# Optimization experiments

Measured on AMD Instinct MI355X. Metric: run time of the kernel, lower is better.

Reference implementation:

```python
import jax, jax.numpy as jnp
import numpy as np

B, LAT, D = 64, 256, 64           # batch, latent dim, voxel grid side (== output image side)
ALPHA_ADJ = float(np.log2(D) + 2)  # alpha_adjust = log2(output_img_shape[0]) + 2


def _rotmat(a):
    """3x3 rotation matrix from Euler angles (x,y,z), R = Rz @ Ry @ Rx."""
    cx, sx = jnp.cos(a[0]), jnp.sin(a[0])
    cy, sy = jnp.cos(a[1]), jnp.sin(a[1])
    cz, sz = jnp.cos(a[2]), jnp.sin(a[2])
    Rx = jnp.array([[1, 0, 0], [0, 0, 0], [0, 0, 0]], jnp.float32).at[1, 1].set(cx).at[1, 2].set(-sx).at[2, 1].set(sx).at[2, 2].set(cx)
    Ry = jnp.array([[0, 0, 0], [0, 1, 0], [0, 0, 0]], jnp.float32).at[0, 0].set(cy).at[0, 2].set(sy).at[2, 0].set(-sy).at[2, 2].set(cy)
    Rz = jnp.array([[0, 0, 0], [0, 0, 0], [0, 0, 1]], jnp.float32).at[0, 0].set(cz).at[0, 1].set(-sz).at[1, 0].set(sz).at[1, 1].set(cz)
    return Rz @ Ry @ Rx


def _apply_transform(vol, R):
    """Rotate a [D,D,D] volume about its centre via trilinear sampling, zero padding."""
    d = vol.shape[0]
    c = (d - 1) / 2.0
    idx = jnp.arange(d, dtype=jnp.float32)
    gi, gj, gk = jnp.meshgrid(idx, idx, idx, indexing='ij')
    dst = jnp.stack([gi, gj, gk], axis=-1) - c        # [D,D,D,3]
    src = dst @ R.T + c                                # source coords
    x, y, z = src[..., 0], src[..., 1], src[..., 2]
    x0 = jnp.floor(x); y0 = jnp.floor(y); z0 = jnp.floor(z)
    fx, fy, fz = x - x0, y - y0, z - z0

    def gather(ix, iy, iz):
        valid = (ix >= 0) & (ix < d) & (iy >= 0) & (iy < d) & (iz >= 0) & (iz < d)
        ixc = jnp.clip(ix, 0, d - 1).astype(jnp.int32)
        iyc = jnp.clip(iy, 0, d - 1).astype(jnp.int32)
        izc = jnp.clip(iz, 0, d - 1).astype(jnp.int32)
        return jnp.where(valid, vol[ixc, iyc, izc], 0.0)

    c000 = gather(x0, y0, z0);     c001 = gather(x0, y0, z0 + 1)
    c010 = gather(x0, y0 + 1, z0); c011 = gather(x0, y0 + 1, z0 + 1)
    c100 = gather(x0 + 1, y0, z0); c101 = gather(x0 + 1, y0, z0 + 1)
    c110 = gather(x0 + 1, y0 + 1, z0); c111 = gather(x0 + 1, y0 + 1, z0 + 1)
    c00 = c000 * (1 - fz) + c001 * fz
    c01 = c010 * (1 - fz) + c011 * fz
    c10 = c100 * (1 - fz) + c101 * fz
    c11 = c110 * (1 - fz) + c111 * fz
    c0 = c00 * (1 - fy) + c01 * fy
    c1 = c10 * (1 - fy) + c11 * fy
    return c0 * (1 - fx) + c1 * fx


def setup_inputs() -> dict:
    key = jax.random.key(0)
    k1, k2, k3 = jax.random.split(key, 3)
    encoded = jax.random.normal(k1, (B, LAT), dtype=jnp.float32)
    W = jax.random.normal(k2, (LAT, D * D * D), dtype=jnp.float32) * 0.02
    b = jnp.zeros((D * D * D,), jnp.float32)
    angles = jax.random.uniform(k3, (B, 3), jnp.float32, -np.pi, np.pi)
    return {"encoded": encoded, "W": W, "b": b, "angles": angles}


def reference(encoded, W, b, angles):
    # voxel_generator: linear -> sigmoid -> [B, D, D, D], then alpha sharpening
    voxels = jax.nn.sigmoid(encoded @ W + b).reshape(B, D, D, D)
    voxels = voxels ** ALPHA_ADJ
    R = jax.vmap(_rotmat)(angles)                       # [B,3,3]
    views = jax.vmap(_apply_transform)(voxels, R)       # [B,D,D,D]
    # alpha compositing back-to-front along last (depth) axis
    alphas = jnp.moveaxis(views, -1, 0)[:, :, None]     # [Dz, B, 1, H, W]
    def step(img, a):
        return img * (1 - a) + a, None
    images, _ = jax.lax.scan(step, jnp.zeros((B, 1, D, D), jnp.float32), alphas, reverse=True)
    return 2 * images - 1
```

## Files before the change

### kernel.cpp

```cpp
#include <hip/hip_runtime.h>
#include <hip/hip_bf16.h>
#include <hip/hip_fp16.h>
#include <math.h>

#define BATCH 64
#define LAT   256
#define DVOX  64
#define VOX   (DVOX*DVOX*DVOX)

typedef __attribute__((ext_vector_type(8))) short short8;
typedef __attribute__((ext_vector_type(4))) float f32x4;

__global__ void prep_kernel(const float* __restrict__ enc,
                            const float* __restrict__ angles,
                            unsigned short* __restrict__ encB,
                            float* __restrict__ Rmat) {
    int tid = threadIdx.x;
    for (int idx = tid; idx < BATCH * LAT; idx += blockDim.x) {
        __hip_bfloat16 h = __float2bfloat16(enc[idx]);
        encB[idx] = *reinterpret_cast<unsigned short*>(&h);
    }
    if (tid < BATCH) {
        float ax = angles[tid*3+0], ay = angles[tid*3+1], az = angles[tid*3+2];
        float cx = cosf(ax), sx = sinf(ax);
        float cy = cosf(ay), sy = sinf(ay);
        float cz = cosf(az), sz = sinf(az);
        float* R = Rmat + tid * 9;
        R[0] = cz*cy;  R[1] = cz*sy*sx - sz*cx;  R[2] = cz*sy*cx + sz*sx;
        R[3] = sz*cy;  R[4] = sz*sy*sx + cz*cx;  R[5] = sz*sy*cx - cz*sx;
        R[6] = -sy;    R[7] = cy*sx;             R[8] = cy*cx;
    }
}

__global__ __launch_bounds__(256, 2) void gemm_mfma_kernel(
        const unsigned short* __restrict__ encB,
        const float* __restrict__ W,
        const float* __restrict__ bias,
        __half* __restrict__ vox) {
    int wave = threadIdx.x >> 6;
    int lane = threadIdx.x & 63;
    int l15 = lane & 15, l4 = lane >> 4;
    int n4 = blockIdx.x * 256 + wave * 64 + 4 * l15;

    f32x4 acc[4][4];
#pragma unroll
    for (int t = 0; t < 4; ++t)
#pragma unroll
        for (int mt = 0; mt < 4; ++mt) acc[t][mt] = (f32x4){0.f, 0.f, 0.f, 0.f};

    const unsigned short* ap = encB + l15 * LAT + l4 * 8;
    const float* wp = W + (size_t)(l4 * 8) * VOX + n4;

    float4 wc[8], wn[8];
#pragma unroll
    for (int j = 0; j < 8; ++j)
        wc[j] = *(const float4*)(wp + (size_t)j * VOX);

#pragma unroll
    for (int kb = 0; kb < LAT; kb += 32) {
        if (kb + 32 < LAT) {
            const float* wpn = wp + (size_t)(kb + 32) * VOX;
#pragma unroll
            for (int j = 0; j < 8; ++j)
                wn[j] = *(const float4*)(wpn + (size_t)j * VOX);
        }
        short8 a[4];
#pragma unroll
        for (int mt = 0; mt < 4; ++mt)
            a[mt] = *(const short8*)(ap + mt * 16 * LAT + kb);

        short8 bf[4];
#pragma unroll
        for (int t = 0; t < 4; ++t) {
#pragma unroll
            for (int dw = 0; dw < 4; ++dw) {
                __hip_bfloat16 lo = __float2bfloat16(wc[2 * dw][t]);
                __hip_bfloat16 hi = __float2bfloat16(wc[2 * dw + 1][t]);
                bf[t][2 * dw]     = *reinterpret_cast<short*>(&lo);
                bf[t][2 * dw + 1] = *reinterpret_cast<short*>(&hi);
            }
        }
#pragma unroll
        for (int t = 0; t < 4; ++t)
#pragma unroll
            for (int mt = 0; mt < 4; ++mt)
                acc[t][mt] = __builtin_amdgcn_mfma_f32_16x16x32_bf16(a[mt], bf[t], acc[t][mt], 0, 0, 0);
#pragma unroll
        for (int j = 0; j < 8; ++j) wc[j] = wn[j];
    }

    float4 bv = *(const float4*)(bias + n4);
#pragma unroll
    for (int mt = 0; mt < 4; ++mt) {
#pragma unroll
        for (int r = 0; r < 4; ++r) {
            int b = mt * 16 + l4 * 4 + r;
            float s[4];
#pragma unroll
            for (int t = 0; t < 4; ++t) {
                float x = acc[t][mt][r] + ((const float*)&bv)[t];
                float v = 1.f / (1.f + __expf(-x));
                v = v * v; v = v * v; v = v * v;
                s[t] = v;
            }
            __half2 h01 = __floats2half2_rn(s[0], s[1]);
            __half2 h23 = __floats2half2_rn(s[2], s[3]);
            uint2 pk;
            pk.x = *reinterpret_cast<unsigned*>(&h01);
            pk.y = *reinterpret_cast<unsigned*>(&h23);
            *reinterpret_cast<uint2*>(vox + (size_t)b * VOX + n4) = pk;
        }
    }
}

__device__ __forceinline__ float zlerp(unsigned e, float fz) {
    __half2 h = *reinterpret_cast<__half2*>(&e);
    float2 f = __half22float2(h);
    return f.x + (f.y - f.x) * fz;
}

__global__ __launch_bounds__(256) void render_lds_kernel(
        const __half* __restrict__ vox,
        const float* __restrict__ Rmat,
        float* __restrict__ out) {
    __shared__ unsigned sV[16 * 16 * 17];
    __shared__ float sT[4][64], sE[4][64];

    int bid  = blockIdx.x;
    int b    = bid & 63;
    int tile = bid >> 6;
    int t    = threadIdx.x;
    int pix  = t & 63, seg = t >> 6;
    int i0 = (tile >> 3) * 8, j0 = (tile & 7) * 8;
    int i = i0 + (pix >> 3);
    int j = j0 + (pix & 7);

    const float* Rb = Rmat + b * 9;
    float R0 = Rb[0], R1 = Rb[1], R2 = Rb[2];
    float R3 = Rb[3], R4 = Rb[4], R5 = Rb[5];
    float R6 = Rb[6], R7 = Rb[7], R8 = Rb[8];

    const float c = (DVOX - 1) * 0.5f;
    float di = (float)i - c, dj = (float)j - c;
    float xb = fmaf(R0, di, fmaf(R1, dj, c));
    float yb = fmaf(R3, di, fmaf(R4, dj, c));
    float zb = fmaf(R6, di, fmaf(R7, dj, c));

    float dic = (float)i0 + 3.5f - c;
    float djc = (float)j0 + 3.5f - c;
    float hwx = 3.5f * (fabsf(R0) + fabsf(R1) + fabsf(R2)) + 1e-3f;
    float hwy = 3.5f * (fabsf(R3) + fabsf(R4) + fabsf(R5)) + 1e-3f;
    float hwz = 3.5f * (fabsf(R6) + fabsf(R7) + fabsf(R8)) + 1e-3f;

    const unsigned short* V = (const unsigned short*)vox + (size_t)b * VOX;

    int rx = t >> 4, ry = t & 15;
    unsigned d[9];
    int xlo_n, ylo_n, zlo_n, s_n;

    auto bbox = [&](int ch) {
        float dkc = (float)(ch * 8) + 3.5f - c;
        float xc = fmaf(R0, dic, fmaf(R1, djc, fmaf(R2, dkc, c)));
        float yc = fmaf(R3, dic, fmaf(R4, djc, fmaf(R5, dkc, c)));
        float zc = fmaf(R6, dic, fmaf(R7, djc, fmaf(R8, dkc, c)));
        xlo_n = (int)floorf(xc - hwx);
        ylo_n = (int)floorf(yc - hwy);
        zlo_n = (int)floorf(zc - hwz);
        s_n   = zlo_n & ~1;
    };
    auto issue = [&]() {
        int gxc = min(max(xlo_n + rx, 0), DVOX - 1);
        int gyc = min(max(ylo_n + ry, 0), DVOX - 1);
        const unsigned* p = (const unsigned*)(V + ((gxc << 12) + (gyc << 6) + s_n));
#pragma unroll
        for (int k = 0; k < 9; ++k) d[k] = p[k];
    };

    bbox(7); issue();
    int xlo = xlo_n, ylo = ylo_n, zlo = zlo_n, s = s_n;

    float img = 0.f;
#pragma unroll 1
    for (int ch = 7; ch >= 0; --ch) {
        bool zint = (zlo >= 0) && (zlo + 17 <= DVOX);

        {
            bool rv = ((unsigned)(xlo + rx) < (unsigned)DVOX) &
                      ((unsigned)(ylo + ry) < (unsigned)DVOX);
            unsigned tt[9];
#pragma unroll
            for (int k = 0; k < 9; ++k) tt[k] = d[k];
            if (!zint) {
#pragma unroll
                for (int k = 0; k < 9; ++k) {
                    int h0 = s + 2 * k;
                    unsigned m = (((unsigned)h0 < (unsigned)DVOX) ? 0x0000FFFFu : 0u)
                               | (((unsigned)(h0 + 1) < (unsigned)DVOX) ? 0xFFFF0000u : 0u);
                    tt[k] &= m;
                }
            }
            unsigned rvm = rv ? 0xFFFFFFFFu : 0u;
#pragma unroll
            for (int k = 0; k < 9; ++k) tt[k] &= rvm;

            unsigned A[8];
#pragma unroll
            for (int m = 0; m < 8; ++m)
                A[m] = (tt[m] >> 16) | (tt[m + 1] << 16);

            unsigned* wrow = sV + t * 17;
            if (zlo & 1) {
#pragma unroll
                for (int m = 0; m < 8; ++m) {
                    wrow[2 * m]     = A[m];
                    wrow[2 * m + 1] = tt[m + 1];
                }
            } else {
#pragma unroll
                for (int m = 0; m < 8; ++m) {
                    wrow[2 * m]     = tt[m];
                    wrow[2 * m + 1] = A[m];
                }
            }
        }
        __syncthreads();

        if (ch > 0) { bbox(ch - 1); issue(); }

        float T = 1.f, E = 0.f;
        int k0 = ch * 8;
#pragma unroll
        for (int q = 1; q >= 0; --q) {
            int kk = 2 * seg + q;
            float dk = (float)(k0 + kk) - c;
            float x = fmaf(R2, dk, xb);
            float y = fmaf(R5, dk, yb);
            float z = fmaf(R8, dk, zb);

            float xf = floorf(x), yf = floorf(y), zf = floorf(z);
            float fx = x - xf, fy = y - yf, fz = z - zf;
            int xi = (int)xf - xlo;
            int yi = (int)yf - ylo;
            int zi = (int)zf - zlo;
            const unsigned* e = sV + (xi * 272 + yi * 17 + zi);

            float c00 = zlerp(e[0],   fz);
            float c01 = zlerp(e[17],  fz);
            float c10 = zlerp(e[272], fz);
            float c11 = zlerp(e[289], fz);
            float c0 = c00 + (c01 - c00) * fy;
            float c1 = c10 + (c11 - c10) * fy;
            float a  = c0  + (c1  - c0 ) * fx;

            E = E * (1.f - a) + a;
            T *= (1.f - a);
        }
        sT[seg][pix] = T;
        sE[seg][pix] = E;
        __syncthreads();

        if (seg == 0) {
            float im = img;
#pragma unroll
            for (int ss = 3; ss >= 0; --ss)
                im = fmaf(sT[ss][pix], im, sE[ss][pix]);
            img = im;
        }

        xlo = xlo_n; ylo = ylo_n; zlo = zlo_n; s = s_n;
    }

    if (seg == 0)
        out[b * (DVOX * DVOX) + i * DVOX + j] = 2.f * img - 1.f;
}

extern "C" void kernel_launch(void* const* d_in, const int* in_sizes, int n_in,
                              void* d_out, int out_size, void* d_ws, size_t ws_size,
                              hipStream_t stream) {
    const float* enc    = (const float*)d_in[0];
    const float* W      = (const float*)d_in[1];
    const float* bias   = (const float*)d_in[2];
    const float* angles = (const float*)d_in[3];
    float* out = (float*)d_out;

    char* ws = (char*)d_ws;
    unsigned short* encB = (unsigned short*)ws;
    float* Rmat          = (float*)(ws + 32768);
    __half* vox          = (__half*)(ws + 65536);

    prep_kernel<<<1, 256, 0, stream>>>(enc, angles, encB, Rmat);
    gemm_mfma_kernel<<<VOX / 256, 256, 0, stream>>>(encB, W, bias, vox);
    render_lds_kernel<<<BATCH * 64, 256, 0, stream>>>(vox, Rmat, out);
}
```

Measured before the change: 143.0 us.

## Coalesce voxel tile loads across lanes and ping-pong W prefetch in GEMM

In the render kernel, each thread used to load 9 strided dwords for one row. Now 4 adjacent lanes split each row: each lane does a uint2 load plus a cross-lane shuffle for the neighbour dword, covering 4 rows per thread, which gives coalesced global access. The next chunk's load is now issued before the barrier. The GEMM kernel replaces the wc/wn copy with A/B ping-pong buffers and uses a cheaper bit-trick bf16 conversion (add 0x8000 then perm), which differs from round-to-nearest-even on ties. These changes add shuffle and predication overhead and alter register pressure.

```diff
diff --git a/kernel.cpp b/kernel.cpp
--- a/kernel.cpp
+++ b/kernel.cpp
@@ -51,42 +51,49 @@
     const unsigned short* ap = encB + l15 * LAT + l4 * 8;
     const float* wp = W + (size_t)(l4 * 8) * VOX + n4;
 
-    float4 wc[8], wn[8];
+    float4 wA[8], wB[8];
 #pragma unroll
     for (int j = 0; j < 8; ++j)
-        wc[j] = *(const float4*)(wp + (size_t)j * VOX);
-
-#pragma unroll
-    for (int kb = 0; kb < LAT; kb += 32) {
-        if (kb + 32 < LAT) {
-            const float* wpn = wp + (size_t)(kb + 32) * VOX;
-#pragma unroll
-            for (int j = 0; j < 8; ++j)
-                wn[j] = *(const float4*)(wpn + (size_t)j * VOX);
-        }
+        wA[j] = *(const float4*)(wp + (size_t)j * VOX);
+
+    auto consume = [&](const float4* w, int kb) {
         short8 a[4];
 #pragma unroll
         for (int mt = 0; mt < 4; ++mt)
             a[mt] = *(const short8*)(ap + mt * 16 * LAT + kb);
-
         short8 bf[4];
 #pragma unroll
         for (int t = 0; t < 4; ++t) {
+            unsigned bw[4];
 #pragma unroll
             for (int dw = 0; dw < 4; ++dw) {
-                __hip_bfloat16 lo = __float2bfloat16(wc[2 * dw][t]);
-                __hip_bfloat16 hi = __float2bfloat16(wc[2 * dw + 1][t]);
-                bf[t][2 * dw]     = *reinterpret_cast<short*>(&lo);
-                bf[t][2 * dw + 1] = *reinterpret_cast<short*>(&hi);
+                unsigned u0 = __float_as_uint(((const float*)&w[2 * dw])[t])     + 0x8000u;
+                unsigned u1 = __float_as_uint(((const float*)&w[2 * dw + 1])[t]) + 0x8000u;
+                bw[dw] = __builtin_amdgcn_perm(u1, u0, 0x07060302u);
             }
+            bf[t] = *reinterpret_cast<short8*>(bw);
         }
 #pragma unroll
         for (int t = 0; t < 4; ++t)
 #pragma unroll
             for (int mt = 0; mt < 4; ++mt)
                 acc[t][mt] = __builtin_amdgcn_mfma_f32_16x16x32_bf16(a[mt], bf[t], acc[t][mt], 0, 0, 0);
-#pragma unroll
-        for (int j = 0; j < 8; ++j) wc[j] = wn[j];
+    };
+
+#pragma unroll
+    for (int kb2 = 0; kb2 < LAT; kb2 += 64) {
+        {
+            const float* q = wp + (size_t)(kb2 + 32) * VOX;
+#pragma unroll
+            for (int j = 0; j < 8; ++j) wB[j] = *(const float4*)(q + (size_t)j * VOX);
+        }
+        consume(wA, kb2);
+        if (kb2 + 64 < LAT) {
+            const float* q = wp + (size_t)(kb2 + 64) * VOX;
+#pragma unroll
+            for (int j = 0; j < 8; ++j) wA[j] = *(const float4*)(q + (size_t)j * VOX);
+        }
+        consume(wB, kb2 + 32);
     }
 
     float4 bv = *(const float4*)(bias + n4);
@@ -130,7 +137,9 @@
     int b    = bid & 63;
     int tile = bid >> 6;
     int t    = threadIdx.x;
+    int lane = t & 63;
     int pix  = t & 63, seg = t >> 6;
+    int m    = t & 3,  rq  = t >> 2;
     int i0 = (tile >> 3) * 8, j0 = (tile & 7) * 8;
     int i = i0 + (pix >> 3);
     int j = j0 + (pix & 7);
@@ -154,8 +163,7 @@
 
     const unsigned short* V = (const unsigned short*)vox + (size_t)b * VOX;
 
-    int rx = t >> 4, ry = t & 15;
-    unsigned d[9];
+    unsigned D0[4], D1[4], D2[4];
     int xlo_n, ylo_n, zlo_n, s_n;
 
     auto bbox = [&](int ch) {
@@ -169,11 +177,17 @@
         s_n   = zlo_n & ~1;
     };
     auto issue = [&]() {
-        int gxc = min(max(xlo_n + rx, 0), DVOX - 1);
-        int gyc = min(max(ylo_n + ry, 0), DVOX - 1);
-        const unsigned* p = (const unsigned*)(V + ((gxc << 12) + (gyc << 6) + s_n));
-#pragma unroll
-        for (int k = 0; k < 9; ++k) d[k] = p[k];
+#pragma unroll
+        for (int p = 0; p < 4; ++p) {
+            int r = 64 * p + rq;
+            int rx = r >> 4, ry = r & 15;
+            int gxc = min(max(xlo_n + rx, 0), DVOX - 1);
+            int gyc = min(max(ylo_n + ry, 0), DVOX - 1);
+            const unsigned* pp = (const unsigned*)V + ((gxc << 11) + (gyc << 5) + (s_n >> 1));
+            uint2 dd = *(const uint2*)(pp + 2 * m);
+            D0[p] = dd.x; D1[p] = dd.y;
+            if (m == 3) D2[p] = pp[8];
+        }
     };
 
     bbox(7); issue();
@@ -183,49 +197,38 @@
 #pragma unroll 1
     for (int ch = 7; ch >= 0; --ch) {
         bool zint = (zlo >= 0) && (zlo + 17 <= DVOX);
-
-        {
+        int  odd  = zlo & 1;
+
+#pragma unroll
+        for (int p = 0; p < 4; ++p) {
+            int r = 64 * p + rq;
+            int rx = r >> 4, ry = r & 15;
             bool rv = ((unsigned)(xlo + rx) < (unsigned)DVOX) &
                       ((unsigned)(ylo + ry) < (unsigned)DVOX);
-            unsigned tt[9];
-#pragma unroll
-            for (int k = 0; k < 9; ++k) tt[k] = d[k];
+            unsigned d0 = D0[p], d1 = D1[p];
+            unsigned dnb = __shfl(D0[p], (lane + 1) & 63);
+            unsigned dn = (m == 3) ? D2[p] : dnb;
             if (!zint) {
-#pragma unroll
-                for (int k = 0; k < 9; ++k) {
-                    int h0 = s + 2 * k;
-                    unsigned m = (((unsigned)h0 < (unsigned)DVOX) ? 0x0000FFFFu : 0u)
-                               | (((unsigned)(h0 + 1) < (unsigned)DVOX) ? 0xFFFF0000u : 0u);
-                    tt[k] &= m;
-                }
+                auto mz = [&](int off) {
+                    int h0 = s + 2 * off;
+                    return (((unsigned)h0 < (unsigned)DVOX) ? 0x0000FFFFu : 0u)
+                         | (((unsigned)(h0 + 1) < (unsigned)DVOX) ? 0xFFFF0000u : 0u);
+                };
+                d0 &= mz(2 * m); d1 &= mz(2 * m + 1); dn &= mz(2 * m + 2);
             }
             unsigned rvm = rv ? 0xFFFFFFFFu : 0u;
-#pragma unroll
-            for (int k = 0; k < 9; ++k) tt[k] &= rvm;
-
-            unsigned A[8];
-#pragma unroll
-            for (int m = 0; m < 8; ++m)
-                A[m] = (tt[m] >> 16) | (tt[m + 1] << 16);
-
-            unsigned* wrow = sV + t * 17;
-            if (zlo & 1) {
-#pragma unroll
-                for (int m = 0; m < 8; ++m) {
-                    wrow[2 * m]     = A[m];
-                    wrow[2 * m + 1] = tt[m + 1];
-                }
-            } else {
-#pragma unroll
-                for (int m = 0; m < 8; ++m) {
-                    wrow[2 * m]     = tt[m];
-                    wrow[2 * m + 1] = A[m];
-                }
-            }
-        }
+            d0 &= rvm; d1 &= rvm; dn &= rvm;
+
+            unsigned A0 = (d0 >> 16) | (d1 << 16);
+            unsigned A1 = (d1 >> 16) | (dn << 16);
+
+            unsigned* wrow = sV + r * 17 + 4 * m;
+            if (odd) { wrow[0] = A0; wrow[1] = d1; wrow[2] = A1; wrow[3] = dn; }
+            else     { wrow[0] = d0; wrow[1] = A0; wrow[2] = d1; wrow[3] = A1; }
+        }
+
+        if (ch > 0) { bbox(ch - 1); issue(); }
         __syncthreads();
-
-        if (ch > 0) { bbox(ch - 1); issue(); }
 
         float T = 1.f, E = 0.f;
         int k0 = ch * 8;
```

Result: slower. 148.9 us (+4.1%).

## Halve GEMM per-thread tile, raise occupancy, use bit-trick bf16 conversion

Applied to the files above, without the earlier changes.

The GEMM kernel now gives each thread 2 output columns instead of 4, doubling the grid and raising the launch-bounds occupancy target from 2 to 4 blocks per CU. W loads are double-buffered in two alternating register sets across an unrolled k loop. The fp32-to-bf16 conversion becomes an add-and-byte-permute round-half-up trick in place of the library conversion. The smaller tile cuts register pressure so more waves can hide the memory-bound W stream, at the cost of narrower float2 loads and re-reading the A operand more often.

```diff
diff --git a/kernel.cpp b/kernel.cpp
--- a/kernel.cpp
+++ b/kernel.cpp
@@ -32,7 +32,7 @@
     }
 }
 
-__global__ __launch_bounds__(256, 2) void gemm_mfma_kernel(
+__global__ __launch_bounds__(256, 4) void gemm_mfma_kernel(
         const unsigned short* __restrict__ encB,
         const float* __restrict__ W,
         const float* __restrict__ bias,
@@ -40,75 +40,77 @@
     int wave = threadIdx.x >> 6;
     int lane = threadIdx.x & 63;
     int l15 = lane & 15, l4 = lane >> 4;
-    int n4 = blockIdx.x * 256 + wave * 64 + 4 * l15;
-
-    f32x4 acc[4][4];
-#pragma unroll
-    for (int t = 0; t < 4; ++t)
+    int n2 = blockIdx.x * 128 + wave * 32 + 2 * l15;
+
+    f32x4 acc[2][4];
+#pragma unroll
+    for (int t = 0; t < 2; ++t)
 #pragma unroll
         for (int mt = 0; mt < 4; ++mt) acc[t][mt] = (f32x4){0.f, 0.f, 0.f, 0.f};
 
     const unsigned short* ap = encB + l15 * LAT + l4 * 8;
-    const float* wp = W + (size_t)(l4 * 8) * VOX + n4;
-
-    float4 wc[8], wn[8];
+    const float* wp = W + (size_t)(l4 * 8) * VOX + n2;
+
+    float2 wA[8], wB[8];
 #pragma unroll
     for (int j = 0; j < 8; ++j)
-        wc[j] = *(const float4*)(wp + (size_t)j * VOX);
-
-#pragma unroll
-    for (int kb = 0; kb < LAT; kb += 32) {
-        if (kb + 32 < LAT) {
-            const float* wpn = wp + (size_t)(kb + 32) * VOX;
-#pragma unroll
-            for (int j = 0; j < 8; ++j)
-                wn[j] = *(const float4*)(wpn + (size_t)j * VOX);
-        }
+        wA[j] = *(const float2*)(wp + (size_t)j * VOX);
+
+    auto consume = [&](const float2* w, int kb) {
         short8 a[4];
 #pragma unroll
         for (int mt = 0; mt < 4; ++mt)
             a[mt] = *(const short8*)(ap + mt * 16 * LAT + kb);
-
-        short8 bf[4];
-#pragma unroll
-        for (int t = 0; t < 4; ++t) {
-#pragma unroll
-            for (int dw = 0; dw < 4; ++dw) {
-                __hip_bfloat16 lo = __float2bfloat16(wc[2 * dw][t]);
-                __hip_bfloat16 hi = __float2bfloat16(wc[2 * dw + 1][t]);
-                bf[t][2 * dw]     = *reinterpret_cast<short*>(&lo);
-                bf[t][2 * dw + 1] = *reinterpret_cast<short*>(&hi);
-            }
-        }
-#pragma unroll
-        for (int t = 0; t < 4; ++t)
-#pragma unroll
-            for (int mt = 0; mt < 4; ++mt)
-                acc[t][mt] = __builtin_amdgcn_mfma_f32_16x16x32_bf16(a[mt], bf[t], acc[t][mt], 0, 0, 0);
-#pragma unroll
-        for (int j = 0; j < 8; ++j) wc[j] = wn[j];
-    }
-
-    float4 bv = *(const float4*)(bias + n4);
+        unsigned bw0[4], bw1[4];
+#pragma unroll
+        for (int dw = 0; dw < 4; ++dw) {
+            unsigned e0 = __float_as_uint(w[2 * dw].x)     + 0x8000u;
+            unsigned e1 = __float_as_uint(w[2 * dw + 1].x) + 0x8000u;
+            bw0[dw] = __builtin_amdgcn_perm(e1, e0, 0x07060302u);
+            unsigned o0 = __float_as_uint(w[2 * dw].y)     + 0x8000u;
+            unsigned o1 = __float_as_uint(w[2 * dw + 1].y) + 0x8000u;
+            bw1[dw] = __builtin_amdgcn_perm(o1, o0, 0x07060302u);
+        }
+        short8 b0 = *reinterpret_cast<short8*>(bw0);
+        short8 b1 = *reinterpret_cast<short8*>(bw1);
+#pragma unroll
+        for (int mt = 0; mt < 4; ++mt) {
+            acc[0][mt] = __builtin_amdgcn_mfma_f32_16x16x32_bf16(a[mt], b0, acc[0][mt], 0, 0, 0);
+            acc[1][mt] = __builtin_amdgcn_mfma_f32_16x16x32_bf16(a[mt], b1, acc[1][mt], 0, 0, 0);
+        }
+    };
+
+#pragma unroll
+    for (int kb2 = 0; kb2 < LAT; kb2 += 64) {
+        {
+            const float* q = wp + (size_t)(kb2 + 32) * VOX;
+#pragma unroll
+            for (int j = 0; j < 8; ++j) wB[j] = *(const float2*)(q + (size_t)j * VOX);
+        }
+        consume(wA, kb2);
+        if (kb2 + 64 < LAT) {
+            const float* q = wp + (size_t)(kb2 + 64) * VOX;
+#pragma unroll
+            for (int j = 0; j < 8; ++j) wA[j] = *(const float2*)(q + (size_t)j * VOX);
+        }
+        consume(wB, kb2 + 32);
+    }
+
+    float2 bv = *(const float2*)(bias + n2);
 #pragma unroll
     for (int mt = 0; mt < 4; ++mt) {
 #pragma unroll
         for (int r = 0; r < 4; ++r) {
             int b = mt * 16 + l4 * 4 + r;
-            float s[4];
-#pragma unroll
-            for (int t = 0; t < 4; ++t) {
-                float x = acc[t][mt][r] + ((const float*)&bv)[t];
-                float v = 1.f / (1.f + __expf(-x));
-                v = v * v; v = v * v; v = v * v;
-                s[t] = v;
-            }
-            __half2 h01 = __floats2half2_rn(s[0], s[1]);
-            __half2 h23 = __floats2half2_rn(s[2], s[3]);
-            uint2 pk;
-            pk.x = *reinterpret_cast<unsigned*>(&h01);
-            pk.y = *reinterpret_cast<unsigned*>(&h23);
-            *reinterpret_cast<uint2*>(vox + (size_t)b * VOX + n4) = pk;
+            float x0 = acc[0][mt][r] + bv.x;
+            float x1 = acc[1][mt][r] + bv.y;
+            float s0 = 1.f / (1.f + __expf(-x0));
+            float s1 = 1.f / (1.f + __expf(-x1));
+            s0 = s0 * s0; s0 = s0 * s0; s0 = s0 * s0;
+            s1 = s1 * s1; s1 = s1 * s1; s1 = s1 * s1;
+            __half2 h01 = __floats2half2_rn(s0, s1);
+            *reinterpret_cast<unsigned*>(vox + (size_t)b * VOX + n2) =
+                *reinterpret_cast<unsigned*>(&h01);
         }
     }
 }
@@ -289,6 +291,6 @@
     __half* vox          = (__half*)(ws + 65536);
 
     prep_kernel<<<1, 256, 0, stream>>>(enc, angles, encB, Rmat);
-    gemm_mfma_kernel<<<VOX / 256, 256, 0, stream>>>(encB, W, bias, vox);
+    gemm_mfma_kernel<<<VOX / 128, 256, 0, stream>>>(encB, W, bias, vox);
     render_lds_kernel<<<BATCH * 64, 256, 0, stream>>>(vox, Rmat, out);
 }
```

Result: slower. 152.1 us (+6.4%).
